# Optimization experiments

Hardware: AMD Instinct MI355X
Metric: run time of the kernel (lower is better)

Reference implementation:

```python
import jax, jax.numpy as jnp
import numpy as np

N = 50000        # node_num
E = 1600000      # num edges (avg degree 32)
IN_DIM = 128
OUT_DIM = 64
SLOPE = 0.1      # leaky relu slope_ratio
EPS = 1e-12


def setup_inputs() -> dict:
    key = jax.random.key(0)
    k0, k1, k2, k3 = jax.random.split(key, 4)
    x = jax.random.normal(k0, (N, IN_DIM), dtype=jnp.float32)
    edge_index = jax.random.randint(k1, (2, E), 0, N, dtype=jnp.int64)
    # Linear(in_dim, out_dim) params
    W = jax.random.normal(k2, (OUT_DIM, IN_DIM), dtype=jnp.float32) * (1.0 / np.sqrt(IN_DIM))
    b = jnp.zeros((OUT_DIM,), dtype=jnp.float32)
    # attention vector a: [2*out_dim, 1], kaiming-normal-ish init
    a = jax.random.normal(k3, (2 * OUT_DIM, 1), dtype=jnp.float32) * np.sqrt(2.0 / (2 * OUT_DIM))
    return {"x": x, "edge_index": edge_index, "W": W, "b": b, "a": a}


def reference(x, edge_index, W, b, a):
    # new_embeddings = Linear(x)
    new = x @ W.T + b                          # [N, OUT_DIM]
    src = edge_index[0]
    dst = edge_index[1]
    # cat(new[src], new[dst]) @ a  ==  new[src]@a_src + new[dst]@a_dst (avoids [E, 2*OUT] intermediate)
    a_src = a[:OUT_DIM, 0]                     # [OUT_DIM]
    a_dst = a[OUT_DIM:, 0]                     # [OUT_DIM]
    score = new[src] @ a_src + new[dst] @ a_dst  # [E]
    e = jnp.exp(jax.nn.leaky_relu(score, SLOPE))  # [E]
    # spmm(A, ones) -> per-row sum of edge weights; spmm(A, new) -> weighted aggregation
    row_sum = jax.ops.segment_sum(e, src, num_segments=N)                 # [N]
    results = jax.ops.segment_sum(e[:, None] * new[dst], src, num_segments=N)  # [N, OUT_DIM]
    return results / (row_sum[:, None] + EPS)
```

## Files before the change

### kernel.cpp

```cpp
#include <hip/hip_runtime.h>
#include <hip/hip_bf16.h>

#define NN    50000
#define EE    1600000
#define IND   128
#define OUTD  64
#define SLOPE 0.1f

#define BSH    5
#define BW     32
#define NB     1564
#define NFINE  1568
#define CAP    1408
#define CAPT   6
#define CSH    8
#define NC     196
#define CAP1   8832
#define NBLK1  500
#define CHUNK1 (EE / NBLK1)
#define NSPLIT 4
#define SCAP   (CAP1 / NSPLIT)

__global__ __launch_bounds__(256) void linear_kernel(
    const float* __restrict__ x, const float* __restrict__ W,
    const float* __restrict__ bias, const float* __restrict__ a,
    ushort* __restrict__ nbuf2, float* __restrict__ s_src, float* __restrict__ s_dst)
{
    __shared__ float Wt[IND][OUTD + 4];
    __shared__ float xs[16][IND + 4];
    const int tid = threadIdx.x;

    #pragma unroll
    for (int i = 0; i < 32; ++i) {
        int idx = tid + i * 256;
        Wt[idx & 127][idx >> 7] = W[idx];
    }
    const int node0 = blockIdx.x * 16;
    const float4* x4 = (const float4*)(x + (size_t)node0 * IND);
    #pragma unroll
    for (int i = 0; i < 2; ++i) {
        int idx = tid + i * 256;
        int row = idx >> 5, col = (idx & 31) * 4;
        *(float4*)&xs[row][col] = x4[idx];
    }
    __syncthreads();

    const int nl = tid >> 4;
    const int jg = tid & 15;
    const int j0 = jg * 4;
    float4 acc = *(const float4*)&bias[j0];
    const float* xrow = xs[nl];
    #pragma unroll
    for (int k = 0; k < IND; k += 4) {
        float4 xv = *(const float4*)&xrow[k];
        float4 w0 = *(const float4*)&Wt[k + 0][j0];
        float4 w1 = *(const float4*)&Wt[k + 1][j0];
        float4 w2 = *(const float4*)&Wt[k + 2][j0];
        float4 w3 = *(const float4*)&Wt[k + 3][j0];
        acc.x = fmaf(xv.x, w0.x, acc.x); acc.y = fmaf(xv.x, w0.y, acc.y);
        acc.z = fmaf(xv.x, w0.z, acc.z); acc.w = fmaf(xv.x, w0.w, acc.w);
        acc.x = fmaf(xv.y, w1.x, acc.x); acc.y = fmaf(xv.y, w1.y, acc.y);
        acc.z = fmaf(xv.y, w1.z, acc.z); acc.w = fmaf(xv.y, w1.w, acc.w);
        acc.x = fmaf(xv.z, w2.x, acc.x); acc.y = fmaf(xv.z, w2.y, acc.y);
        acc.z = fmaf(xv.z, w2.z, acc.z); acc.w = fmaf(xv.z, w2.w, acc.w);
        acc.x = fmaf(xv.w, w3.x, acc.x); acc.y = fmaf(xv.w, w3.y, acc.y);
        acc.z = fmaf(xv.w, w3.z, acc.z); acc.w = fmaf(xv.w, w3.w, acc.w);
    }
    const int n = node0 + nl;
    ushort4 pk;
    { __hip_bfloat16 h;
      h = __float2bfloat16(acc.x); pk.x = *(ushort*)&h;
      h = __float2bfloat16(acc.y); pk.y = *(ushort*)&h;
      h = __float2bfloat16(acc.z); pk.z = *(ushort*)&h;
      h = __float2bfloat16(acc.w); pk.w = *(ushort*)&h; }
    *(ushort4*)&nbuf2[(size_t)n * OUTD + j0] = pk;

    float ss = acc.x * a[j0]        + acc.y * a[j0 + 1]
             + acc.z * a[j0 + 2]    + acc.w * a[j0 + 3];
    float sd = acc.x * a[OUTD + j0]     + acc.y * a[OUTD + j0 + 1]
             + acc.z * a[OUTD + j0 + 2] + acc.w * a[OUTD + j0 + 3];
    #pragma unroll
    for (int m = 1; m < 16; m <<= 1) {
        ss += __shfl_xor(ss, m, 64);
        sd += __shfl_xor(sd, m, 64);
    }
    if (jg == 0) { s_src[n] = ss; s_dst[n] = sd; }
}

__global__ __launch_bounds__(256) void coarsebin_kernel(const int* __restrict__ ei,
                                                        int* __restrict__ gcur1,
                                                        unsigned* __restrict__ ebuf1)
{
    __shared__ int h[NC];
    for (int i = threadIdx.x; i < NC; i += 256) h[i] = 0;
    __syncthreads();
    const int base = blockIdx.x * CHUNK1;
    const int4* s4p = (const int4*)(ei + base);
    for (int i = threadIdx.x; i < CHUNK1 / 4; i += 256) {
        int4 s4 = s4p[i];
        atomicAdd(&h[s4.x >> CSH], 1);
        atomicAdd(&h[s4.y >> CSH], 1);
        atomicAdd(&h[s4.z >> CSH], 1);
        atomicAdd(&h[s4.w >> CSH], 1);
    }
    __syncthreads();
    for (int i = threadIdx.x; i < NC; i += 256) {
        int c = h[i];
        if (c) h[i] = i * CAP1 + atomicAdd(&gcur1[i * 16], c);
    }
    __syncthreads();
    const int4* d4p = (const int4*)(ei + EE + base);
    for (int i = threadIdx.x; i < CHUNK1 / 4; i += 256) {
        int4 s4 = s4p[i];
        int4 d4 = d4p[i];
        int p0 = atomicAdd(&h[s4.x >> CSH], 1);
        int p1 = atomicAdd(&h[s4.y >> CSH], 1);
        int p2 = atomicAdd(&h[s4.z >> CSH], 1);
        int p3 = atomicAdd(&h[s4.w >> CSH], 1);
        ebuf1[p0] = ((unsigned)(s4.x & 255) << 16) | (unsigned)d4.x;
        ebuf1[p1] = ((unsigned)(s4.y & 255) << 16) | (unsigned)d4.y;
        ebuf1[p2] = ((unsigned)(s4.z & 255) << 16) | (unsigned)d4.z;
        ebuf1[p3] = ((unsigned)(s4.w & 255) << 16) | (unsigned)d4.w;
    }
}

__global__ __launch_bounds__(256) void finebin_kernel(
    const unsigned* __restrict__ ebuf1, const int* __restrict__ gcur1,
    int* __restrict__ gcur2, unsigned* __restrict__ ebuf2)
{
    __shared__ unsigned stage[SCAP];
    __shared__ int h[8], lofs[8], grun[8], cur[8];
    const int tid = threadIdx.x;
    const int c   = blockIdx.x >> 2;
    const int sp  = blockIdx.x & 3;
    const int cnt1 = gcur1[c * 16];
    const int seg  = (cnt1 + NSPLIT - 1) / NSPLIT;
    const int lo   = sp * seg;
    const int m    = max(0, min(cnt1, lo + seg) - lo);
    if (tid < 8) h[tid] = 0;
    __syncthreads();
    const unsigned* eb = ebuf1 + (size_t)c * CAP1 + lo;
    for (int i = tid; i < m; i += 256)
        atomicAdd(&h[eb[i] >> 21], 1);
    __syncthreads();
    if (tid == 0) {
        int run = 0;
        #pragma unroll
        for (int f = 0; f < 8; ++f) { lofs[f] = run; run += h[f]; }
    }
    __syncthreads();
    if (tid < 8) {
        cur[tid]  = lofs[tid];
        grun[tid] = atomicAdd(&gcur2[(c * 8 + tid) * 16], h[tid]);
    }
    __syncthreads();
    for (int i = tid; i < m; i += 256) {
        unsigned e = eb[i];
        int pos = atomicAdd(&cur[e >> 21], 1);
        stage[pos] = (((e >> 16) & 31u) << 16) | (e & 0xFFFFu);
    }
    __syncthreads();
    #pragma unroll 1
    for (int f = 0; f < 8; ++f) {
        const int cf = h[f];
        unsigned* dst = ebuf2 + (size_t)(c * 8 + f) * CAP + grun[f];
        const unsigned* sp2 = stage + lofs[f];
        for (int i = tid; i < cf; i += 256) dst[i] = sp2[i];
    }
}

__global__ __launch_bounds__(256) void aggregate_kernel(
    const unsigned* __restrict__ ebuf, const int* __restrict__ gcur,
    const ushort* __restrict__ nbuf2,
    const float* __restrict__ s_src, const float* __restrict__ s_dst,
    float* __restrict__ out)
{
    __shared__ uint2 pairs[CAP];
    __shared__ float ssL[BW];
    __shared__ int cntL[BW], ofs[BW], cur[BW];
    const int tid  = threadIdx.x;
    const int wid  = tid >> 6;
    const int lane = tid & 63;
    const int b    = blockIdx.x;
    const int n0   = b << BSH;

    if (tid < BW) {
        int n = n0 + tid;
        ssL[tid]  = (n < NN) ? s_src[n] : 0.f;
        cntL[tid] = 0;
    }
    __syncthreads();

    const int cnt = gcur[b * 16];
    const unsigned* eb = ebuf + (size_t)b * CAP;

    unsigned er[CAPT]; float evr[CAPT];
    int nk = 0;
    for (int i = tid; i < cnt; i += 256) {
        unsigned e = eb[i];
        int d  = e & 0xFFFFu;
        int ln = e >> 16;
        float sc = ssL[ln] + s_dst[d];
        float lr = sc > 0.f ? sc : SLOPE * sc;
        er[nk] = e; evr[nk] = __expf(lr); ++nk;
        atomicAdd(&cntL[ln], 1);
    }
    __syncthreads();

    if (wid == 0) {
        int c = (lane < BW) ? cntL[lane] : 0;
        int sc = c;
        #pragma unroll
        for (int m = 1; m < BW; m <<= 1) {
            int v = __shfl_up(sc, m, 64);
            if (lane >= m) sc += v;
        }
        if (lane < BW) { ofs[lane] = sc - c; cur[lane] = sc - c; }
    }
    __syncthreads();

    for (int k = 0; k < nk; ++k) {
        int ln = er[k] >> 16;
        int pos = atomicAdd(&cur[ln], 1);
        pairs[pos] = make_uint2(er[k] & 0xFFFFu, __float_as_uint(evr[k]));
    }
    __syncthreads();

    #pragma unroll 1
    for (int t = 0; t < BW / 4; ++t) {
        const int ln  = wid * (BW / 4) + t;
        const int beg = ofs[ln];
        const int len = cntL[ln];

        float acc = 0.f, es = 0.f;
        int j = 0;
        for (; j + 8 <= len; j += 8) {
            uint2 p0 = pairs[beg + j + 0], p1 = pairs[beg + j + 1];
            uint2 p2 = pairs[beg + j + 2], p3 = pairs[beg + j + 3];
            uint2 p4 = pairs[beg + j + 4], p5 = pairs[beg + j + 5];
            uint2 p6 = pairs[beg + j + 6], p7 = pairs[beg + j + 7];
            ushort u0 = nbuf2[(size_t)p0.x * OUTD + lane];
            ushort u1 = nbuf2[(size_t)p1.x * OUTD + lane];
            ushort u2 = nbuf2[(size_t)p2.x * OUTD + lane];
            ushort u3 = nbuf2[(size_t)p3.x * OUTD + lane];
            ushort u4 = nbuf2[(size_t)p4.x * OUTD + lane];
            ushort u5 = nbuf2[(size_t)p5.x * OUTD + lane];
            ushort u6 = nbuf2[(size_t)p6.x * OUTD + lane];
            ushort u7 = nbuf2[(size_t)p7.x * OUTD + lane];
            float f0 = __uint_as_float(p0.y), f1 = __uint_as_float(p1.y);
            float f2 = __uint_as_float(p2.y), f3 = __uint_as_float(p3.y);
            float f4 = __uint_as_float(p4.y), f5 = __uint_as_float(p5.y);
            float f6 = __uint_as_float(p6.y), f7 = __uint_as_float(p7.y);
            es += f0 + f1 + f2 + f3 + f4 + f5 + f6 + f7;
            acc = fmaf(f0, __uint_as_float((unsigned)u0 << 16), acc);
            acc = fmaf(f1, __uint_as_float((unsigned)u1 << 16), acc);
            acc = fmaf(f2, __uint_as_float((unsigned)u2 << 16), acc);
            acc = fmaf(f3, __uint_as_float((unsigned)u3 << 16), acc);
            acc = fmaf(f4, __uint_as_float((unsigned)u4 << 16), acc);
            acc = fmaf(f5, __uint_as_float((unsigned)u5 << 16), acc);
            acc = fmaf(f6, __uint_as_float((unsigned)u6 << 16), acc);
            acc = fmaf(f7, __uint_as_float((unsigned)u7 << 16), acc);
        }
        for (; j < len; ++j) {
            uint2 p = pairs[beg + j];
            ushort u = nbuf2[(size_t)p.x * OUTD + lane];
            float f = __uint_as_float(p.y);
            es += f;
            acc = fmaf(f, __uint_as_float((unsigned)u << 16), acc);
        }
        const int n = n0 + ln;
        if (n < NN)
            out[(size_t)n * OUTD + lane] = acc / (es + 1e-12f);
    }
}

extern "C" void kernel_launch(void* const* d_in, const int* in_sizes, int n_in,
                              void* d_out, int out_size, void* d_ws, size_t ws_size,
                              hipStream_t stream) {
    const float* x  = (const float*)d_in[0];
    const int*   ei = (const int*)d_in[1];
    const float* W  = (const float*)d_in[2];
    const float* b  = (const float*)d_in[3];
    const float* a  = (const float*)d_in[4];
    float* out = (float*)d_out;

    ushort*   nbuf2 = (ushort*)d_ws;
    float*    s_src = (float*)(nbuf2 + (size_t)NN * OUTD);
    float*    s_dst = s_src + NN;
    int*      gcur1 = (int*)(s_dst + NN);
    int*      gcur2 = gcur1 + NC * 16;
    unsigned* ebuf1 = (unsigned*)(gcur2 + NFINE * 16);
    unsigned* ebuf2 = ebuf1 + (size_t)NC * CAP1;

    hipMemsetAsync(gcur1, 0, (NC + NFINE) * 16 * sizeof(int), stream);
    linear_kernel<<<NN / 16, 256, 0, stream>>>(x, W, b, a, nbuf2, s_src, s_dst);
    coarsebin_kernel<<<NBLK1, 256, 0, stream>>>(ei, gcur1, ebuf1);
    finebin_kernel<<<NC * NSPLIT, 256, 0, stream>>>(ebuf1, gcur1, gcur2, ebuf2);
    aggregate_kernel<<<NB, 256, 0, stream>>>(ebuf2, gcur2, nbuf2, s_src, s_dst, out);
}
```

Measured before the change: 176.5 us.

## Use bf16 MFMA for linear projection and split-edge dword gathers in aggregation

The linear kernel now converts x and W to bf16 in shared memory and computes the projection with 16x16x32 bf16 MFMA instructions instead of scalar FP32 FMAs, staging results through shared memory for the bf16 store and score reduction. The aggregate kernel now has each half-wave handle alternate edges and gather 32-bit words (two bf16 features) per lane, then combines the two halves with a cross-lane shuffle before writing float2 outputs. This is meant to cut ALU cost in the GEMM and to halve the number of gather instructions per edge. The cost is extra precision loss from rounding x and W to bf16, plus some shuffle overhead.

```diff
diff --git a/kernel.cpp b/kernel.cpp
--- a/kernel.cpp
+++ b/kernel.cpp
@@ -21,64 +21,82 @@
 #define NSPLIT 4
 #define SCAP   (CAP1 / NSPLIT)
 
+typedef __attribute__((ext_vector_type(8))) short short8;
+typedef __attribute__((ext_vector_type(4))) float float4v;
+
 __global__ __launch_bounds__(256) void linear_kernel(
     const float* __restrict__ x, const float* __restrict__ W,
     const float* __restrict__ bias, const float* __restrict__ a,
     ushort* __restrict__ nbuf2, float* __restrict__ s_src, float* __restrict__ s_dst)
 {
-    __shared__ float Wt[IND][OUTD + 4];
-    __shared__ float xs[16][IND + 4];
+    __shared__ ushort xs[16 * 136];
+    __shared__ ushort wt[64 * 136];
+    __shared__ float  newt[16 * 68];
     const int tid = threadIdx.x;
-
-    #pragma unroll
-    for (int i = 0; i < 32; ++i) {
+    const int node0 = blockIdx.x * 16;
+
+    const float4* W4 = (const float4*)W;
+    #pragma unroll
+    for (int i = 0; i < 8; ++i) {
         int idx = tid + i * 256;
-        Wt[idx & 127][idx >> 7] = W[idx];
-    }
-    const int node0 = blockIdx.x * 16;
+        float4 wv = W4[idx];
+        int n = idx >> 5, k = (idx & 31) * 4;
+        ushort4 pk; __hip_bfloat16 h;
+        h = __float2bfloat16(wv.x); pk.x = *(ushort*)&h;
+        h = __float2bfloat16(wv.y); pk.y = *(ushort*)&h;
+        h = __float2bfloat16(wv.z); pk.z = *(ushort*)&h;
+        h = __float2bfloat16(wv.w); pk.w = *(ushort*)&h;
+        *(ushort4*)&wt[n * 136 + k] = pk;
+    }
     const float4* x4 = (const float4*)(x + (size_t)node0 * IND);
     #pragma unroll
     for (int i = 0; i < 2; ++i) {
         int idx = tid + i * 256;
-        int row = idx >> 5, col = (idx & 31) * 4;
-        *(float4*)&xs[row][col] = x4[idx];
-    }
+        float4 xv = x4[idx];
+        int r = idx >> 5, cc = (idx & 31) * 4;
+        ushort4 pk; __hip_bfloat16 h;
+        h = __float2bfloat16(xv.x); pk.x = *(ushort*)&h;
+        h = __float2bfloat16(xv.y); pk.y = *(ushort*)&h;
+        h = __float2bfloat16(xv.z); pk.z = *(ushort*)&h;
+        h = __float2bfloat16(xv.w); pk.w = *(ushort*)&h;
+        *(ushort4*)&xs[r * 136 + cc] = pk;
+    }
+    __syncthreads();
+
+    const int w    = tid >> 6;
+    const int lane = tid & 63;
+    const int q    = lane >> 4;
+    const int m16  = lane & 15;
+    float4v acc = {0.f, 0.f, 0.f, 0.f};
+    #pragma unroll
+    for (int kk = 0; kk < IND; kk += 32) {
+        short8 af = *(const short8*)&xs[m16 * 136 + kk + q * 8];
+        short8 bf = *(const short8*)&wt[(w * 16 + m16) * 136 + kk + q * 8];
+        acc = __builtin_amdgcn_mfma_f32_16x16x32_bf16(af, bf, acc, 0, 0, 0);
+    }
+    const float bv = bias[w * 16 + m16];
+    #pragma unroll
+    for (int r = 0; r < 4; ++r)
+        newt[(q * 4 + r) * 68 + w * 16 + m16] = acc[r] + bv;
     __syncthreads();
 
     const int nl = tid >> 4;
     const int jg = tid & 15;
     const int j0 = jg * 4;
-    float4 acc = *(const float4*)&bias[j0];
-    const float* xrow = xs[nl];
-    #pragma unroll
-    for (int k = 0; k < IND; k += 4) {
-        float4 xv = *(const float4*)&xrow[k];
-        float4 w0 = *(const float4*)&Wt[k + 0][j0];
-        float4 w1 = *(const float4*)&Wt[k + 1][j0];
-        float4 w2 = *(const float4*)&Wt[k + 2][j0];
-        float4 w3 = *(const float4*)&Wt[k + 3][j0];
-        acc.x = fmaf(xv.x, w0.x, acc.x); acc.y = fmaf(xv.x, w0.y, acc.y);
-        acc.z = fmaf(xv.x, w0.z, acc.z); acc.w = fmaf(xv.x, w0.w, acc.w);
-        acc.x = fmaf(xv.y, w1.x, acc.x); acc.y = fmaf(xv.y, w1.y, acc.y);
-        acc.z = fmaf(xv.y, w1.z, acc.z); acc.w = fmaf(xv.y, w1.w, acc.w);
-        acc.x = fmaf(xv.z, w2.x, acc.x); acc.y = fmaf(xv.z, w2.y, acc.y);
-        acc.z = fmaf(xv.z, w2.z, acc.z); acc.w = fmaf(xv.z, w2.w, acc.w);
-        acc.x = fmaf(xv.w, w3.x, acc.x); acc.y = fmaf(xv.w, w3.y, acc.y);
-        acc.z = fmaf(xv.w, w3.z, acc.z); acc.w = fmaf(xv.w, w3.w, acc.w);
-    }
+    float4 va = *(const float4*)&newt[nl * 68 + j0];
     const int n = node0 + nl;
     ushort4 pk;
     { __hip_bfloat16 h;
-      h = __float2bfloat16(acc.x); pk.x = *(ushort*)&h;
-      h = __float2bfloat16(acc.y); pk.y = *(ushort*)&h;
-      h = __float2bfloat16(acc.z); pk.z = *(ushort*)&h;
-      h = __float2bfloat16(acc.w); pk.w = *(ushort*)&h; }
+      h = __float2bfloat16(va.x); pk.x = *(ushort*)&h;
+      h = __float2bfloat16(va.y); pk.y = *(ushort*)&h;
+      h = __float2bfloat16(va.z); pk.z = *(ushort*)&h;
+      h = __float2bfloat16(va.w); pk.w = *(ushort*)&h; }
     *(ushort4*)&nbuf2[(size_t)n * OUTD + j0] = pk;
 
-    float ss = acc.x * a[j0]        + acc.y * a[j0 + 1]
-             + acc.z * a[j0 + 2]    + acc.w * a[j0 + 3];
-    float sd = acc.x * a[OUTD + j0]     + acc.y * a[OUTD + j0 + 1]
-             + acc.z * a[OUTD + j0 + 2] + acc.w * a[OUTD + j0 + 3];
+    float ss = va.x * a[j0]        + va.y * a[j0 + 1]
+             + va.z * a[j0 + 2]    + va.w * a[j0 + 3];
+    float sd = va.x * a[OUTD + j0]     + va.y * a[OUTD + j0 + 1]
+             + va.z * a[OUTD + j0 + 2] + va.w * a[OUTD + j0 + 3];
     #pragma unroll
     for (int m = 1; m < 16; m <<= 1) {
         ss += __shfl_xor(ss, m, 64);
@@ -183,6 +201,7 @@
     const int lane = tid & 63;
     const int b    = blockIdx.x;
     const int n0   = b << BSH;
+    const unsigned* __restrict__ nbuf4 = (const unsigned*)nbuf2;
 
     if (tid < BW) {
         int n = n0 + tid;
@@ -226,51 +245,56 @@
     }
     __syncthreads();
 
+    const int h32 = lane >> 5;
+    const int c32 = lane & 31;
+
     #pragma unroll 1
     for (int t = 0; t < BW / 4; ++t) {
         const int ln  = wid * (BW / 4) + t;
         const int beg = ofs[ln];
         const int len = cntL[ln];
 
-        float acc = 0.f, es = 0.f;
+        float accL = 0.f, accH = 0.f, es = 0.f;
         int j = 0;
         for (; j + 8 <= len; j += 8) {
-            uint2 p0 = pairs[beg + j + 0], p1 = pairs[beg + j + 1];
-            uint2 p2 = pairs[beg + j + 2], p3 = pairs[beg + j + 3];
-            uint2 p4 = pairs[beg + j + 4], p5 = pairs[beg + j + 5];
-            uint2 p6 = pairs[beg + j + 6], p7 = pairs[beg + j + 7];
-            ushort u0 = nbuf2[(size_t)p0.x * OUTD + lane];
-            ushort u1 = nbuf2[(size_t)p1.x * OUTD + lane];
-            ushort u2 = nbuf2[(size_t)p2.x * OUTD + lane];
-            ushort u3 = nbuf2[(size_t)p3.x * OUTD + lane];
-            ushort u4 = nbuf2[(size_t)p4.x * OUTD + lane];
-            ushort u5 = nbuf2[(size_t)p5.x * OUTD + lane];
-            ushort u6 = nbuf2[(size_t)p6.x * OUTD + lane];
-            ushort u7 = nbuf2[(size_t)p7.x * OUTD + lane];
-            float f0 = __uint_as_float(p0.y), f1 = __uint_as_float(p1.y);
-            float f2 = __uint_as_float(p2.y), f3 = __uint_as_float(p3.y);
-            float f4 = __uint_as_float(p4.y), f5 = __uint_as_float(p5.y);
-            float f6 = __uint_as_float(p6.y), f7 = __uint_as_float(p7.y);
-            es += f0 + f1 + f2 + f3 + f4 + f5 + f6 + f7;
-            acc = fmaf(f0, __uint_as_float((unsigned)u0 << 16), acc);
-            acc = fmaf(f1, __uint_as_float((unsigned)u1 << 16), acc);
-            acc = fmaf(f2, __uint_as_float((unsigned)u2 << 16), acc);
-            acc = fmaf(f3, __uint_as_float((unsigned)u3 << 16), acc);
-            acc = fmaf(f4, __uint_as_float((unsigned)u4 << 16), acc);
-            acc = fmaf(f5, __uint_as_float((unsigned)u5 << 16), acc);
-            acc = fmaf(f6, __uint_as_float((unsigned)u6 << 16), acc);
-            acc = fmaf(f7, __uint_as_float((unsigned)u7 << 16), acc);
+            uint2 pA = pairs[beg + j + 0 + h32];
+            uint2 pB = pairs[beg + j + 2 + h32];
+            uint2 pC = pairs[beg + j + 4 + h32];
+            uint2 pD = pairs[beg + j + 6 + h32];
+            unsigned gA = nbuf4[pA.x * 32 + c32];
+            unsigned gB = nbuf4[pB.x * 32 + c32];
+            unsigned gC = nbuf4[pC.x * 32 + c32];
+            unsigned gD = nbuf4[pD.x * 32 + c32];
+            float fA = __uint_as_float(pA.y), fB = __uint_as_float(pB.y);
+            float fC = __uint_as_float(pC.y), fD = __uint_as_float(pD.y);
+            es += fA + fB + fC + fD;
+            accL = fmaf(fA, __uint_as_float(gA << 16), accL);
+            accH = fmaf(fA, __uint_as_float(gA & 0xFFFF0000u), accH);
+            accL = fmaf(fB, __uint_as_float(gB << 16), accL);
+            accH = fmaf(fB, __uint_as_float(gB & 0xFFFF0000u), accH);
+            accL = fmaf(fC, __uint_as_float(gC << 16), accL);
+            accH = fmaf(fC, __uint_as_float(gC & 0xFFFF0000u), accH);
+            accL = fmaf(fD, __uint_as_float(gD << 16), accL);
+            accH = fmaf(fD, __uint_as_float(gD & 0xFFFF0000u), accH);
         }
-        for (; j < len; ++j) {
-            uint2 p = pairs[beg + j];
-            ushort u = nbuf2[(size_t)p.x * OUTD + lane];
-            float f = __uint_as_float(p.y);
+        for (; j < len; j += 2) {
+            int idx = j + h32;
+            uint2 p = pairs[beg + min(idx, len - 1)];
+            float f = (idx < len) ? __uint_as_float(p.y) : 0.f;
+            unsigned g = nbuf4[p.x * 32 + c32];
             es += f;
-            acc = fmaf(f, __uint_as_float((unsigned)u << 16), acc);
+            accL = fmaf(f, __uint_as_float(g << 16), accL);
+            accH = fmaf(f, __uint_as_float(g & 0xFFFF0000u), accH);
         }
+        es   += __shfl_xor(es, 32, 64);
+        accL += __shfl_xor(accL, 32, 64);
+        accH += __shfl_xor(accH, 32, 64);
         const int n = n0 + ln;
-        if (n < NN)
-            out[(size_t)n * OUTD + lane] = acc / (es + 1e-12f);
+        if (h32 == 0 && n < NN) {
+            float inv = 1.f / (es + 1e-12f);
+            float2 o = make_float2(accL * inv, accH * inv);
+            *(float2*)&out[(size_t)n * OUTD + 2 * c32] = o;
+        }
     }
 }
 
```

New measurement: 150.5 us. 1.17x faster.
